# Optimization experiments

Measured on AMD Instinct MI355X. Metric: run time of the kernel, lower is better.

Reference implementation:

```python
import jax, jax.numpy as jnp
import numpy as np
from jax import lax


def setup_inputs() -> dict:
    key = jax.random.key(0)
    ks = jax.random.split(key, 6)
    B, T, D = 8, 2048, 1024  # d_inner == dim (expansion=1.0)
    scale = 1.0 / np.sqrt(D)
    return {
        "x": jax.random.normal(ks[0], (B, T, D), dtype=jnp.float32),
        "h0": jnp.zeros((B, D), dtype=jnp.float32),
        "W_in": jax.random.normal(ks[1], (D, D), dtype=jnp.float32) * scale,
        "W_x": jax.random.normal(ks[2], (D, D), dtype=jnp.float32) * scale,
        "alpha_raw": jnp.full((D,), -2.0, dtype=jnp.float32),
        "b": jnp.zeros((D,), dtype=jnp.float32),
        "b_gate": jnp.zeros((D,), dtype=jnp.float32),
        "W_out": jax.random.normal(ks[3], (D, D), dtype=jnp.float32) * scale,
    }


def reference(x, h0, W_in, W_x, alpha_raw, b, b_gate, W_out):
    # x: [B, T, dim]
    x_proj = jnp.einsum('btd,ed->bte', x, W_in)          # in_proj, no bias
    x_rnn = jnp.transpose(x_proj, (1, 0, 2))             # [T, B, Di]
    alpha = jax.nn.sigmoid(alpha_raw)                    # [Di]
    xw = jnp.einsum('tbd,ed->tbe', x_rnn, W_x)           # precompute W_x @ x_t

    def step(h_prev, inputs):
        xw_t, xr_t = inputs
        h_new = jnp.tanh(xw_t + alpha * h_prev + b)
        out_t = h_new * jax.nn.silu(xr_t + b_gate)       # x-only SiLU gate
        return h_new, out_t

    h_final, cell_out = lax.scan(step, h0, (xw, x_rnn))  # cell_out: [T, B, Di]
    cell_out = jnp.transpose(cell_out, (1, 0, 2))        # [B, T, Di]
    output = jnp.einsum('bte,de->btd', cell_out, W_out)  # out_proj, no bias
    return output, h_final
```

## Files before the change

### kernel.cpp

```cpp
#include <hip/hip_runtime.h>
#include <hip/hip_bf16.h>
#include <stdint.h>


typedef __bf16 bf16x8 __attribute__((ext_vector_type(8)));
typedef float  f32x4  __attribute__((ext_vector_type(4)));

__device__ __forceinline__ unsigned short f2bf(float f) {
  uint32_t u = __float_as_uint(f);
  uint32_t r = (u + 0x7FFFu + ((u >> 16) & 1u)) >> 16;
  return (unsigned short)r;
}
__device__ __forceinline__ float bf2f(uint32_t h) {
  return __uint_as_float(h << 16);
}
__device__ __forceinline__ float tanh_fast(float x) {
  float e = __expf(2.0f * x);
  return 1.0f - 2.0f / (e + 1.0f);
}

__global__ __launch_bounds__(256) void frag_f32(
    const float* __restrict__ W, unsigned short* __restrict__ out, int K, int KB) {
  const int u = blockIdx.x * 256 + threadIdx.x;
  const int lane = u & 63;
  const int grp  = u >> 6;
  const int n = (grp / KB) * 16 + (lane & 15);
  const int k = (grp % KB) * 32 + ((lane >> 4) & 3) * 8;
  const float4* p = (const float4*)(W + (size_t)n * K + k);
  float4 a = p[0], b = p[1];
  union { unsigned short us[8]; uint4 v; } r;
  r.us[0] = f2bf(a.x); r.us[1] = f2bf(a.y); r.us[2] = f2bf(a.z); r.us[3] = f2bf(a.w);
  r.us[4] = f2bf(b.x); r.us[5] = f2bf(b.y); r.us[6] = f2bf(b.z); r.us[7] = f2bf(b.w);
  *(uint4*)(out + (size_t)u * 8) = r.v;
}

__global__ __launch_bounds__(256) void frag_f32_T(
    const float* __restrict__ W, unsigned short* __restrict__ out, int N, int KB) {
  const int u = blockIdx.x * 256 + threadIdx.x;
  const int lane = u & 63;
  const int grp  = u >> 6;
  const int n = (grp / KB) * 16 + (lane & 15);
  const int k = (grp % KB) * 32 + ((lane >> 4) & 3) * 8;
  union { unsigned short us[8]; uint4 v; } r;
#pragma unroll
  for (int j = 0; j < 8; ++j) r.us[j] = f2bf(W[(size_t)(k + j) * N + n]);
  *(uint4*)(out + (size_t)u * 8) = r.v;
}

__global__ __launch_bounds__(256) void frag_bf16(
    const unsigned short* __restrict__ W, unsigned short* __restrict__ out,
    int K, int KB) {
  const int u = blockIdx.x * 256 + threadIdx.x;
  const int lane = u & 63;
  const int grp  = u >> 6;
  const int n = (grp / KB) * 16 + (lane & 15);
  const int k = (grp % KB) * 32 + ((lane >> 4) & 3) * 8;
  *(uint4*)(out + (size_t)u * 8) = *(const uint4*)(W + (size_t)n * K + k);
}

#define BM 128
#define BN 128

template <int SM>
__global__ __launch_bounds__(256) void gemm_frag(
    const unsigned short* __restrict__ Af, const unsigned short* __restrict__ Bf,
    void* __restrict__ Cv, int M, int N, int K) {
  const int tid  = threadIdx.x;
  const int lane = tid & 63;
  const int wave = tid >> 6;
  const int wrow = wave >> 1;
  const int wcol = wave & 1;
  const int rowBase = blockIdx.x * BM;
  const int colBase = blockIdx.y * BN;
  const int q   = lane >> 4;
  const int r16 = lane & 15;
  const int KB  = K >> 5;

  const unsigned short* ap[4];
  const unsigned short* bp[4];
#pragma unroll
  for (int i = 0; i < 4; ++i) {
    const int rb = (rowBase >> 4) + wrow * 4 + i;
    const int nb = (colBase >> 4) + wcol * 4 + i;
    ap[i] = Af + ((size_t)rb * KB * 64 + lane) * 8;
    bp[i] = Bf + ((size_t)nb * KB * 64 + lane) * 8;
  }

  f32x4 acc[4][4] = {};
  bf16x8 a0[4], b0[4];
#pragma unroll
  for (int i = 0; i < 4; ++i) {
    a0[i] = *(const bf16x8*)ap[i];
    b0[i] = *(const bf16x8*)bp[i];
  }

  for (int kb = 0; kb < KB; ++kb) {
    const size_t noff = (size_t)((kb + 1 < KB) ? kb + 1 : kb) * 512;
    bf16x8 a1[4], b1[4];
#pragma unroll
    for (int i = 0; i < 4; ++i) {
      a1[i] = *(const bf16x8*)(ap[i] + noff);
      b1[i] = *(const bf16x8*)(bp[i] + noff);
    }
#pragma unroll
    for (int i = 0; i < 4; ++i)
#pragma unroll
      for (int j = 0; j < 4; ++j)
        acc[i][j] = __builtin_amdgcn_mfma_f32_16x16x32_bf16(a0[i], b0[j], acc[i][j], 0, 0, 0);
#pragma unroll
    for (int i = 0; i < 4; ++i) { a0[i] = a1[i]; b0[i] = b1[i]; }
  }

#pragma unroll
  for (int i = 0; i < 4; ++i) {
#pragma unroll
    for (int j = 0; j < 4; ++j) {
#pragma unroll
      for (int rg = 0; rg < 4; ++rg) {
        long long row = rowBase + wrow * 64 + i * 16 + q * 4 + rg;
        long long col = colBase + wcol * 64 + j * 16 + r16;
        float v = acc[i][j][rg];
        if (SM == 0) ((float*)Cv)[row * (long long)N + col] = v;
        else ((unsigned short*)Cv)[row * (long long)N + col] = f2bf(v);
      }
    }
  }
}

__global__ __launch_bounds__(256) void scan_kernel2(
    const unsigned short* __restrict__ xcat,
    const float* __restrict__ h0, const float* __restrict__ araw,
    const float* __restrict__ bvec, const float* __restrict__ bgate,
    unsigned short* __restrict__ cell, float* __restrict__ hfin,
    int Bv, int T, int D, int NC, int CH, int WARM) {
  const int idx = blockIdx.x * 256 + threadIdx.x;
  const int D2  = D >> 1;
  const int BD2 = Bv * D2;
  const int c = idx / BD2;
  if (c >= NC) return;
  const int ld2 = idx - c * BD2;
  const int b = ld2 / D2;
  const int d = (ld2 - b * D2) * 2;

  const float2 ar = *(const float2*)&araw[d];
  const float ax = 1.0f / (1.0f + __expf(-ar.x));
  const float ay = 1.0f / (1.0f + __expf(-ar.y));
  const float2 bb = *(const float2*)&bvec[d];
  const float2 bg = *(const float2*)&bgate[d];

  const int tb = c * CH;
  const int te = (tb + CH < T) ? (tb + CH) : T;
  int t0 = tb - WARM;
  float hx, hy;
  if (t0 <= 0) {
    t0 = 0;
    float2 h00 = *(const float2*)&h0[b * D + d];
    hx = h00.x; hy = h00.y;
  } else { hx = 0.0f; hy = 0.0f; }

  const int N2 = 2 * D;
  long long off = ((long long)b * T + t0) * N2 + D + d;
  for (int t = t0; t < tb; ++t) {
    uint32_t w2 = *(const uint32_t*)&xcat[off];
    hx = tanh_fast(__builtin_fmaf(ax, hx, bf2f(w2 & 0xffffu) + bb.x));
    hy = tanh_fast(__builtin_fmaf(ay, hy, bf2f(w2 >> 16) + bb.y));
    off += N2;
  }
  long long offp = ((long long)b * T + tb) * N2 + d;
  const int KBS = D * 16;
  const int dconst = (d >> 5) * 512 + ((d >> 3) & 3) * 128 + (d & 7);
  int m = b * T + tb;
  long long offc = (long long)(m >> 4) * KBS + (m & 15) * 8 + dconst;
  for (int t = tb; t < te; ++t) {
    uint32_t w2 = *(const uint32_t*)&xcat[off];
    uint32_t p2 = *(const uint32_t*)&xcat[offp];
    hx = tanh_fast(__builtin_fmaf(ax, hx, bf2f(w2 & 0xffffu) + bb.x));
    hy = tanh_fast(__builtin_fmaf(ay, hy, bf2f(w2 >> 16) + bb.y));
    float zx = bf2f(p2 & 0xffffu) + bg.x;
    float zy = bf2f(p2 >> 16) + bg.y;
    float ox = hx * zx / (1.0f + __expf(-zx));
    float oy = hy * zy / (1.0f + __expf(-zy));
    *(uint32_t*)&cell[offc] = (uint32_t)f2bf(ox) | ((uint32_t)f2bf(oy) << 16);
    off += N2; offp += N2;
    ++m;
    offc += 8;
    if ((m & 15) == 0) offc += (long long)KBS - 128;
  }
  if (te == T) {
    float2 hv; hv.x = hx; hv.y = hy;
    *(float2*)&hfin[b * D + d] = hv;
  }
}

extern "C" void kernel_launch(void* const* d_in, const int* in_sizes, int n_in,
                              void* d_out, int out_size, void* d_ws, size_t ws_size,
                              hipStream_t stream) {
  const float* x         = (const float*)d_in[0];
  const float* h0        = (const float*)d_in[1];
  const float* W_in      = (const float*)d_in[2];
  const float* W_x       = (const float*)d_in[3];
  const float* alpha_raw = (const float*)d_in[4];
  const float* b         = (const float*)d_in[5];
  const float* b_gate    = (const float*)d_in[6];
  const float* W_out     = (const float*)d_in[7];

  const int D  = in_sizes[4];
  const int BD = in_sizes[1];
  const int Bv = BD / D;
  const int M  = in_sizes[0] / D;
  const int T  = M / Bv;
  const int KB = D >> 5;

  float* out  = (float*)d_out;
  float* hfin = out + (long long)M * D;

  const size_t szXf  = (size_t)M * D * 2;
  const size_t szCat = (size_t)M * D * 4;
  const size_t szW   = (size_t)D * D * 2;

  char* ws = (char*)d_ws;
  unsigned short* xfrag = (unsigned short*)ws; ws += szXf;
  unsigned short* xcat  = (unsigned short*)ws; ws += szCat;
  unsigned short* WcatF = (unsigned short*)ws; ws += 2 * szW;
  unsigned short* WoutF = (unsigned short*)ws; ws += szW;
  unsigned short* WxF    = xcat;
  unsigned short* WinTF  = xcat + (size_t)D * D;
  unsigned short* WcombR = xcat + 2 * (size_t)D * D;
  unsigned short* cell   = xfrag;
  unsigned short* WcombF = WcatF + (size_t)D * D;

  const int xBlocks = (int)((size_t)M * D / 2048);
  const int wBlocks = (int)((size_t)D * D / 2048);

  frag_f32<<<xBlocks, 256, 0, stream>>>(x, xfrag, D, KB);
  frag_f32<<<wBlocks, 256, 0, stream>>>(W_x, WxF, D, KB);
  frag_f32_T<<<wBlocks, 256, 0, stream>>>(W_in, WinTF, D, KB);
  frag_f32<<<wBlocks, 256, 0, stream>>>(W_in, WcatF, D, KB);
  frag_f32<<<wBlocks, 256, 0, stream>>>(W_out, WoutF, D, KB);

  gemm_frag<1><<<dim3(D / BM, D / BN), 256, 0, stream>>>(WxF, WinTF, WcombR, D, D, D);
  frag_bf16<<<wBlocks, 256, 0, stream>>>(WcombR, WcombF, D, KB);

  gemm_frag<1><<<dim3(M / BM, (2 * D) / BN), 256, 0, stream>>>(xfrag, WcatF, xcat, M, 2 * D, D);

  const int CH = 32;
  const int WARM = 16;
  const int NC = (T + CH - 1) / CH;
  const int total2 = NC * (BD >> 1);
  scan_kernel2<<<(total2 + 255) / 256, 256, 0, stream>>>(
      xcat, h0, alpha_raw, b, b_gate, cell, hfin, Bv, T, D, NC, CH, WARM);

  gemm_frag<0><<<dim3(M / BM, D / BN), 256, 0, stream>>>(cell, WoutF, out, M, D, D);
}
```

Measured before the change: 325.8 us.

## Add 256x256-tile GEMM with triple-buffered direct-to-LDS loads for projections

Introduces a new GEMM kernel with 512 threads per block and 256x256 output tiles. It stages pre-fragmented A and B tiles straight into LDS with global_load_lds across three buffers, interleaves the loads with MFMA compute, and raises wave priority around the MFMA bursts. The two large projection GEMMs (input projection and output projection) now use it in place of the older gemm_frag. The aim is more data reuse per tile and better overlap of memory with compute. In exchange it uses 96KB of LDS per block and many accumulator registers, and the large tiles give fewer blocks for the output GEMM.

```diff
diff --git a/kernel.cpp b/kernel.cpp
--- a/kernel.cpp
+++ b/kernel.cpp
@@ -5,6 +5,9 @@
 
 typedef __bf16 bf16x8 __attribute__((ext_vector_type(8)));
 typedef float  f32x4  __attribute__((ext_vector_type(4)));
+
+#define AS1 __attribute__((address_space(1)))
+#define AS3 __attribute__((address_space(3)))
 
 __device__ __forceinline__ unsigned short f2bf(float f) {
   uint32_t u = __float_as_uint(f);
@@ -119,6 +122,119 @@
       for (int rg = 0; rg < 4; ++rg) {
         long long row = rowBase + wrow * 64 + i * 16 + q * 4 + rg;
         long long col = colBase + wcol * 64 + j * 16 + r16;
+        float v = acc[i][j][rg];
+        if (SM == 0) ((float*)Cv)[row * (long long)N + col] = v;
+        else ((unsigned short*)Cv)[row * (long long)N + col] = f2bf(v);
+      }
+    }
+  }
+}
+
+template <int SM>
+__global__ __launch_bounds__(512, 2) void gemm256(
+    const unsigned short* __restrict__ Af, const unsigned short* __restrict__ Bf,
+    void* __restrict__ Cv, int N, int K) {
+  __shared__ __attribute__((aligned(128))) char smem[98304];
+  const int tid  = threadIdx.x;
+  const int lane = tid & 63;
+  const int w    = tid >> 6;
+  const int wr   = w >> 2;
+  const int wc   = w & 3;
+  const int KB   = K >> 5;
+  const int NT   = KB;
+  const int rbBase = blockIdx.x << 4;
+  const int nbBase = blockIdx.y << 4;
+
+  const char* Ab = (const char*)Af;
+  const char* Bb = (const char*)Bf;
+
+  f32x4 acc[8][4] = {};
+
+#define STAGE_A(sb, tt)                                                         \
+  {                                                                             \
+    _Pragma("unroll")                                                           \
+    for (int i_ = 0; i_ < 2; ++i_) {                                            \
+      const int g_ = w * 2 + i_;                                                \
+      const size_t go_ = (((size_t)(rbBase + g_) * KB + (size_t)(tt)) << 10) +  \
+                         (size_t)(lane << 4);                                   \
+      __builtin_amdgcn_global_load_lds((AS1 void*)(Ab + go_),                   \
+          (AS3 void*)(smem + (sb) * 32768 + (g_ << 10)), 16, 0, 0);             \
+    }                                                                           \
+  }
+#define STAGE_B(sb, tt)                                                         \
+  {                                                                             \
+    _Pragma("unroll")                                                           \
+    for (int i_ = 0; i_ < 2; ++i_) {                                            \
+      const int g_ = w * 2 + i_;                                                \
+      const size_t go_ = (((size_t)(nbBase + g_) * KB + (size_t)(tt)) << 10) +  \
+                         (size_t)(lane << 4);                                   \
+      __builtin_amdgcn_global_load_lds((AS1 void*)(Bb + go_),                   \
+          (AS3 void*)(smem + (sb) * 32768 + 16384 + (g_ << 10)), 16, 0, 0);     \
+    }                                                                           \
+  }
+
+  STAGE_A(0, 0); STAGE_B(0, 0);
+  STAGE_A(1, 1); STAGE_B(1, 1);
+  asm volatile("s_waitcnt vmcnt(4)" ::: "memory");
+  asm volatile("s_barrier" ::: "memory");
+
+  int buf = 0;
+  for (int t = 0; t < NT; ++t) {
+    const char* LA = smem + buf * 32768;
+    const char* LB = LA + 16384;
+    const int sbuf = (buf == 0) ? 2 : buf - 1;
+    bf16x8 a[4], b[4], a2[4];
+
+#pragma unroll
+    for (int j = 0; j < 4; ++j)
+      b[j] = *(const bf16x8*)(LB + (((wc << 2) + j) << 10) + (lane << 4));
+#pragma unroll
+    for (int i = 0; i < 4; ++i)
+      a[i] = *(const bf16x8*)(LA + (((wr << 3) + i) << 10) + (lane << 4));
+    if (t + 2 < NT) STAGE_A(sbuf, t + 2);
+    asm volatile("s_barrier" ::: "memory");
+    __builtin_amdgcn_s_setprio(1);
+#pragma unroll
+    for (int i = 0; i < 4; ++i)
+#pragma unroll
+      for (int j = 0; j < 4; ++j)
+        acc[i][j] = __builtin_amdgcn_mfma_f32_16x16x32_bf16(a[i], b[j], acc[i][j], 0, 0, 0);
+    __builtin_amdgcn_s_setprio(0);
+    asm volatile("s_barrier" ::: "memory");
+
+#pragma unroll
+    for (int i = 0; i < 4; ++i)
+      a2[i] = *(const bf16x8*)(LA + (((wr << 3) + 4 + i) << 10) + (lane << 4));
+    if (t + 2 < NT) STAGE_B(sbuf, t + 2);
+    asm volatile("s_barrier" ::: "memory");
+    __builtin_amdgcn_s_setprio(1);
+#pragma unroll
+    for (int i = 0; i < 4; ++i)
+#pragma unroll
+      for (int j = 0; j < 4; ++j)
+        acc[4 + i][j] = __builtin_amdgcn_mfma_f32_16x16x32_bf16(a2[i], b[j], acc[4 + i][j], 0, 0, 0);
+    __builtin_amdgcn_s_setprio(0);
+
+    if (t + 2 < NT) {
+      asm volatile("s_waitcnt vmcnt(4)" ::: "memory");
+    } else if (t + 1 < NT) {
+      asm volatile("s_waitcnt vmcnt(0)" ::: "memory");
+    }
+    asm volatile("s_barrier" ::: "memory");
+    buf = (buf == 2) ? 0 : buf + 1;
+  }
+#undef STAGE_A
+#undef STAGE_B
+
+  const int q = lane >> 4, r16 = lane & 15;
+#pragma unroll
+  for (int i = 0; i < 8; ++i) {
+#pragma unroll
+    for (int j = 0; j < 4; ++j) {
+#pragma unroll
+      for (int rg = 0; rg < 4; ++rg) {
+        long long row = (long long)blockIdx.x * 256 + wr * 128 + i * 16 + q * 4 + rg;
+        long long col = (long long)blockIdx.y * 256 + wc * 64 + j * 16 + r16;
         float v = acc[i][j][rg];
         if (SM == 0) ((float*)Cv)[row * (long long)N + col] = v;
         else ((unsigned short*)Cv)[row * (long long)N + col] = f2bf(v);
@@ -241,7 +357,7 @@
   gemm_frag<1><<<dim3(D / BM, D / BN), 256, 0, stream>>>(WxF, WinTF, WcombR, D, D, D);
   frag_bf16<<<wBlocks, 256, 0, stream>>>(WcombR, WcombF, D, KB);
 
-  gemm_frag<1><<<dim3(M / BM, (2 * D) / BN), 256, 0, stream>>>(xfrag, WcatF, xcat, M, 2 * D, D);
+  gemm256<1><<<dim3(M / 256, (2 * D) / 256), 512, 0, stream>>>(xfrag, WcatF, xcat, 2 * D, D);
 
   const int CH = 32;
   const int WARM = 16;
@@ -250,5 +366,5 @@
   scan_kernel2<<<(total2 + 255) / 256, 256, 0, stream>>>(
       xcat, h0, alpha_raw, b, b_gate, cell, hfin, Bv, T, D, NC, CH, WARM);
 
-  gemm_frag<0><<<dim3(M / BM, D / BN), 256, 0, stream>>>(cell, WoutF, out, M, D, D);
-}
+  gemm256<0><<<dim3(M / 256, D / 256), 512, 0, stream>>>(cell, WoutF, out, M > 0 ? D : D, D);
+}
```

Measured after the change: 300.7 us. 7.7% less time.
